# Performance work log

Hardware: AMD Instinct MI355X
Metric: run time of the kernel (lower is better)

The kernel has to match this reference:

```python
import jax, jax.numpy as jnp
import numpy as np

B, S, D, H, DK, L, DFF, V = 64, 128, 512, 8, 64, 6, 2048, 72
AH = 2          # heads of the internal mask-generating attention encoder (hard-coded n_heads=2)
PRECET = 0.2    # fraction of lowest-attention prefix tokens to mask
NEG = -1e9


def pos_enc(s, d):
    pos = jnp.arange(s, dtype=jnp.float32)[:, None]
    div = jnp.exp(jnp.arange(0, d, 2, dtype=jnp.float32) * (-np.log(10000.0) / d))
    pe = jnp.zeros((s, d), jnp.float32)
    pe = pe.at[:, 0::2].set(jnp.sin(pos * div))
    pe = pe.at[:, 1::2].set(jnp.cos(pos * div))
    return pe


def ln(x, eps=1e-5):  # LayerNorm with default (identity) affine params, as in the source
    m = x.mean(-1, keepdims=True)
    v = ((x - m) ** 2).mean(-1, keepdims=True)
    return (x - m) / jnp.sqrt(v + eps)


def attn_block(x, pad, WQ, WK, WV, WO, heads):
    b, s, _ = x.shape
    dk = WQ.shape[1] // heads
    q = (x @ WQ).reshape(b, s, heads, dk).transpose(0, 2, 1, 3)
    k = (x @ WK).reshape(b, s, heads, dk).transpose(0, 2, 1, 3)
    v = (x @ WV).reshape(b, s, heads, dk).transpose(0, 2, 1, 3)
    scores = jnp.einsum('bhqd,bhkd->bhqk', q, k) / np.sqrt(dk)
    scores = jnp.where(pad[:, None, None, :], NEG, scores)
    attn = jax.nn.softmax(scores, axis=-1)
    ascore = attn.sum(axis=2)                                   # [b, h, s] column sums
    ctx = jnp.einsum('bhqk,bhkd->bqhd', attn, v).reshape(b, s, heads * dk)
    return ln(ctx @ WO + x), attn, ascore


def ffn_block(x, W1, W2):
    return ln(jax.nn.relu(x @ W1) @ W2 + x)


def encode(x, pad, tWQ, tWK, tWV, tFC, tF1, tF2):
    def step(h, p):
        WQ, WK, WV, WO, W1, W2 = p
        h, _, asc = attn_block(h, pad, WQ, WK, WV, WO, H)
        h = ffn_block(h, W1, W2)
        return h, asc.sum(axis=1)                               # sum over heads -> [b, s]
    h, scores = jax.lax.scan(step, x, (tWQ, tWK, tWV, tFC, tF1, tF2))
    return h, scores                                            # scores: [L, b, s]


def creat_mask(col, tokens):
    # col[i, j] == 0 exactly iff token j is pad (softmax of -1e9 underflows to 0).
    b, s = tokens.shape
    iszero = col == 0.0
    has = iszero.any(axis=1)
    j0 = jnp.where(has, jnp.argmax(iszero, axis=1), s)          # first pad position
    kk = jnp.where(has, jnp.ceil(PRECET * j0.astype(jnp.float32)).astype(jnp.int32), 0)
    idx = jnp.arange(s)
    vals = jnp.where(idx[None, :] < j0[:, None], col, jnp.inf)
    ranks = jnp.argsort(jnp.argsort(vals, axis=1), axis=1)      # rank 0 = smallest attention
    keep = (ranks >= kk[:, None]).astype(tokens.dtype)
    return tokens * keep


def pre_head(x, pW1, pb1, pW2, pb2, pW3, pb3):
    x = jax.nn.relu(x @ pW1 + pb1)
    x = jax.nn.relu(x @ pW2 + pb2)
    return x @ pW3 + pb3


def setup_inputs():
    key = jax.random.key(0)
    ks = jax.random.split(key, 18)
    g = lambda k, shp: jax.random.normal(k, shp, jnp.float32) * 0.02
    return {
        'tokens': jax.random.randint(ks[0], (B, S), 0, V, dtype=jnp.int32),
        'emb': g(ks[1], (V, D)),
        'aWQ': g(ks[2], (D, AH * DK)), 'aWK': g(ks[3], (D, AH * DK)), 'aWV': g(ks[4], (D, AH * DK)),
        'aFC': g(ks[5], (AH * DK, D)), 'aF1': g(ks[6], (D, DFF)), 'aF2': g(ks[7], (DFF, D)),
        'tWQ': g(ks[8], (L, D, H * DK)), 'tWK': g(ks[9], (L, D, H * DK)), 'tWV': g(ks[10], (L, D, H * DK)),
        'tFC': g(ks[11], (L, H * DK, D)), 'tF1': g(ks[12], (L, D, DFF)), 'tF2': g(ks[13], (L, DFF, D)),
        'pW1': g(ks[14], (D * S, 1024)), 'pb1': jnp.zeros((1024,), jnp.float32),
        'pW2': g(ks[15], (1024, 512)), 'pb2': jnp.zeros((512,), jnp.float32),
        'pW3': g(ks[16], (512, 128)), 'pb3': jnp.zeros((128,), jnp.float32),
    }


def reference(tokens, emb, aWQ, aWK, aWV, aFC, aF1, aF2,
              tWQ, tWK, tWV, tFC, tF1, tF2,
              pW1, pb1, pW2, pb2, pW3, pb3):
    pe = pos_enc(S, D)[None]
    pad = tokens == 0
    x = emb[tokens] + pe
    # 1-layer / 2-head mask-generating encoder; only its attn matrix is consumed downstream
    _, mattn, _ = attn_block(x, pad, aWQ, aWK, aWV, aFC, AH)
    col = mattn.sum(axis=1).sum(axis=1)                         # heads then queries -> [B, S]
    mtok = creat_mask(col, tokens)
    xm = emb[mtok] + pe
    h, scores = encode(x, pad, tWQ, tWK, tWV, tFC, tF1, tF2)
    hm, _ = encode(xm, mtok == 0, tWQ, tWK, tWV, tFC, tF1, tF2)
    out1 = pre_head(h.reshape(B, -1), pW1, pb1, pW2, pb2, pW3, pb3)
    outm = pre_head(hm.reshape(B, -1), pW1, pb1, pW2, pb2, pW3, pb3)
    return tokens, out1, mtok, outm, scores
```

## Files before the change

kernel.cpp:

```cpp
#include <hip/hip_runtime.h>
#include <hip/hip_bf16.h>
#include <math.h>

using u16 = unsigned short;
using u32 = unsigned int;

constexpr int B   = 64;
constexpr int S   = 128;
constexpr int D   = 512;
constexpr int H   = 8;
constexpr int DK  = 64;
constexpr int L   = 6;
constexpr int DFF = 2048;
constexpr int AH  = 2;
constexpr int BS  = B * S;
constexpr int BS2 = 2 * BS;

constexpr long OUT_TOK    = 0;
constexpr long OUT_OUT1   = 8192;
constexpr long OUT_MTOK   = 16384;
constexpr long OUT_OUTM   = 24576;
constexpr long OUT_SCORES = 32768;

constexpr long OFF_PE   = 0;
constexpr long OFF_ASC  = 65536;
constexpr long OFF_COLP = 196608;
constexpr long OFF_MTOK = 212992;
constexpr long OFF_X    = 221184;
constexpr long OFF_XB   = 8609792;
constexpr long OFF_QB   = 12804096;
constexpr long OFF_KB   = 16998400;
constexpr long OFF_VB   = 21192704;
constexpr long OFF_TB   = 25387008;
constexpr long OFF_W    = 42164224;
constexpr long WSTRIDE  = 3145728;

typedef __attribute__((ext_vector_type(8))) short bf16x8;
typedef __attribute__((ext_vector_type(4))) float f32x4;

__device__ __forceinline__ float b2f(u16 u) {
    union { u32 i; float f; } v; v.i = ((u32)u) << 16; return v.f;
}
__device__ __forceinline__ u16 f2b(float f) {
    union { float f; u32 i; } v; v.f = f;
    u32 r = v.i + 0x7fffu + ((v.i >> 16) & 1u);
    return (u16)(r >> 16);
}

#define GLOAD_LDS16(g, l) __builtin_amdgcn_global_load_lds(                        \
    (const __attribute__((address_space(1))) u32*)(const void*)(g),               \
    (__attribute__((address_space(3))) u32*)(void*)(l), 16, 0, 0)

__global__ void pe_kernel(float* __restrict__ pe) {
    int idx = blockIdx.x * 256 + threadIdx.x;
    if (idx >= S * (D / 2)) return;
    int s = idx >> 8;
    int i = idx & 255;
    const float CPE = (float)(-9.210340371976184 / 512.0);
    float div = expf((float)(2 * i) * CPE);
    float ang = (float)s * div;
    pe[(long)s * D + 2 * i]     = sinf(ang);
    pe[(long)s * D + 2 * i + 1] = cosf(ang);
}

__global__ void embed_dual(const int* __restrict__ toks, const float* __restrict__ emb,
                           const float* __restrict__ pe, float* __restrict__ x,
                           u16* __restrict__ xb) {
    int i8 = blockIdx.x * 256 + threadIdx.x;
    if (i8 >= BS * D / 8) return;
    int row = i8 >> 6;
    int c8  = i8 & 63;
    int s   = row & (S - 1);
    int t   = toks[row];
    float4 e0 = *(const float4*)(emb + (long)t * D + c8 * 8);
    float4 e1 = *(const float4*)(emb + (long)t * D + c8 * 8 + 4);
    float4 p0 = *(const float4*)(pe + (long)s * D + c8 * 8);
    float4 p1 = *(const float4*)(pe + (long)s * D + c8 * 8 + 4);
    float4 o0, o1;
    o0.x = e0.x + p0.x; o0.y = e0.y + p0.y; o0.z = e0.z + p0.z; o0.w = e0.w + p0.w;
    o1.x = e1.x + p1.x; o1.y = e1.y + p1.y; o1.z = e1.z + p1.z; o1.w = e1.w + p1.w;
    *(float4*)(x + (long)i8 * 8)     = o0;
    *(float4*)(x + (long)i8 * 8 + 4) = o1;
    u16 u[8] = {f2b(o0.x), f2b(o0.y), f2b(o0.z), f2b(o0.w), f2b(o1.x), f2b(o1.y), f2b(o1.z), f2b(o1.w)};
    *(uint4*)(xb + (long)i8 * 8) = *(uint4*)u;
}

__global__ __launch_bounds__(256)
void wconv_all(const float* __restrict__ tWQ, const float* __restrict__ tWK,
               const float* __restrict__ tWV, const float* __restrict__ tFC,
               const float* __restrict__ tF1, const float* __restrict__ tF2,
               u16* __restrict__ wAll) {
    __shared__ float t[32][33];
    const int lyr = blockIdx.x / 3072;
    const int bid = blockIdx.x % 3072;
    u16* base = wAll + (long)lyr * WSTRIDE;
    const float* src; u16* dst; int KK, NN, tk, tn;
    if (bid < 1024) {
        int which = bid >> 8, tt = bid & 255;
        src = (which == 0 ? tWQ : which == 1 ? tWK : which == 2 ? tWV : tFC) + (long)lyr * D * D;
        dst = base + (long)which * 262144;
        KK = 512; NN = 512; tk = tt >> 4; tn = tt & 15;
    } else if (bid < 2048) {
        int tt = bid - 1024;
        src = tF1 + (long)lyr * D * DFF; dst = base + 1048576;
        KK = 512; NN = 2048; tk = tt >> 6; tn = tt & 63;
    } else {
        int tt = bid - 2048;
        src = tF2 + (long)lyr * DFF * D; dst = base + 2097152;
        KK = 2048; NN = 512; tk = tt >> 4; tn = tt & 15;
    }
    int ty = threadIdx.x >> 5, tx = threadIdx.x & 31;
    #pragma unroll
    for (int i = 0; i < 4; i++)
        t[ty + i * 8][tx] = src[(long)(tk * 32 + ty + i * 8) * NN + tn * 32 + tx];
    __syncthreads();
    #pragma unroll
    for (int i = 0; i < 4; i++)
        dst[(long)(tn * 32 + ty + i * 8) * KK + tk * 32 + tx] = f2b(t[tx][ty + i * 8]);
}

template<int EPI, int OUTB>
__device__ __forceinline__ void gemm_core(
        const u16* __restrict__ A, const u16* __restrict__ Wt,
        float* C, u16* Cb, const float* __restrict__ X,
        int M, int N, int K, int m0, int n0) {
    __shared__ u16 As[128 * 32];
    __shared__ u16 Bs[128 * 32];
    const int tid = threadIdx.x;
    const int w = tid >> 6, l = tid & 63;
    const int wr = (w >> 1) * 64, wc = (w & 1) * 64;
    f32x4 acc[4][4];
    #pragma unroll
    for (int i = 0; i < 4; i++)
        #pragma unroll
        for (int j = 0; j < 4; j++) { f32x4 z = {0.f, 0.f, 0.f, 0.f}; acc[i][j] = z; }

    const int srow = w * 32 + (l >> 2);
    const int scol = (l & 3) * 8;
    const u16* gA = A + (long)(m0 + srow) * K + scol;
    const u16* gB = Wt + (long)(n0 + srow) * K + scol;
    u16* lA0 = As + w * 1024;
    u16* lA1 = As + w * 1024 + 512;
    u16* lB0 = Bs + w * 1024;
    u16* lB1 = Bs + w * 1024 + 512;

    for (int k0 = 0; k0 < K; k0 += 32) {
        GLOAD_LDS16(gA + k0,               lA0);
        GLOAD_LDS16(gA + (long)16 * K + k0, lA1);
        GLOAD_LDS16(gB + k0,               lB0);
        GLOAD_LDS16(gB + (long)16 * K + k0, lB1);
        __syncthreads();
        bf16x8 aF[4], bF[4];
        #pragma unroll
        for (int mi = 0; mi < 4; mi++)
            aF[mi] = *(const bf16x8*)(As + (wr + mi * 16 + (l & 15)) * 32 + (l >> 4) * 8);
        #pragma unroll
        for (int ni = 0; ni < 4; ni++)
            bF[ni] = *(const bf16x8*)(Bs + (wc + ni * 16 + (l & 15)) * 32 + (l >> 4) * 8);
        #pragma unroll
        for (int mi = 0; mi < 4; mi++)
            #pragma unroll
            for (int ni = 0; ni < 4; ni++)
                acc[mi][ni] = __builtin_amdgcn_mfma_f32_16x16x32_bf16(aF[mi], bF[ni], acc[mi][ni], 0, 0, 0);
        __syncthreads();
    }

    #pragma unroll
    for (int mi = 0; mi < 4; mi++) {
        #pragma unroll
        for (int ni = 0; ni < 4; ni++) {
            const int col = n0 + wc + ni * 16 + (l & 15);
            #pragma unroll
            for (int r = 0; r < 4; r++) {
                const int row = m0 + wr + mi * 16 + (l >> 4) * 4 + r;
                const long idx = (long)row * N + col;
                float v = acc[mi][ni][r];
                if (EPI == 1) v += X[idx];
                if (EPI == 2) v = fmaxf(v, 0.0f);
                if (OUTB) Cb[idx] = f2b(v);
                else      C[idx]  = v;
            }
        }
    }
}

__global__ __launch_bounds__(256)
void gemm_qkv_b(const u16* __restrict__ A, const u16* wq, const u16* wk, const u16* wv,
                u16* qb, u16* kb, u16* vb, int M, int N, int K) {
    const u16* Wt = blockIdx.z == 0 ? wq : blockIdx.z == 1 ? wk : wv;
    u16* Cb       = blockIdx.z == 0 ? qb : blockIdx.z == 1 ? kb : vb;
    gemm_core<0, 1>(A, Wt, nullptr, Cb, nullptr, M, N, K, blockIdx.x * 128, blockIdx.y * 128);
}
__global__ __launch_bounds__(256)
void gemm_relu_b(const u16* __restrict__ A, const u16* __restrict__ Wt,
                 u16* Cb, int M, int N, int K) {
    gemm_core<2, 1>(A, Wt, nullptr, Cb, nullptr, M, N, K, blockIdx.x * 128, blockIdx.y * 128);
}

__global__ __launch_bounds__(512)
void gemm_ln(const u16* __restrict__ A, const u16* __restrict__ Wt,
             float* x, u16* __restrict__ xb, int K) {
    __shared__ u16 As[64 * 32];
    __shared__ u16 Bs[512 * 32];
    __shared__ float redS[64][9];
    __shared__ float redQ[64][9];
    __shared__ float meanS[64], invS[64];
    const int m0 = blockIdx.x * 64;
    const int tid = threadIdx.x;
    const int w = tid >> 6, l = tid & 63;
    const int wc = w * 64;

    f32x4 acc[4][4];
    #pragma unroll
    for (int i = 0; i < 4; i++)
        #pragma unroll
        for (int j = 0; j < 4; j++) { f32x4 z = {0.f, 0.f, 0.f, 0.f}; acc[i][j] = z; }

    const int scol = (l & 3) * 8;
    const u16* gA = A + (long)(m0 + w * 16 + (l >> 2)) * K + scol;
    const u16* gB = Wt + (long)(w * 64 + (l >> 2)) * K + scol;
    u16* lA = As + (w * 16) * 32;
    u16* lB = Bs + (w * 64) * 32;

    for (int k0 = 0; k0 < K; k0 += 32) {
        if (w < 4) GLOAD_LDS16(gA + k0, lA);
        #pragma unroll
        for (int j = 0; j < 4; j++)
            GLOAD_LDS16(gB + (long)j * 16 * K + k0, lB + j * 16 * 32);
        __syncthreads();
        bf16x8 aF[4], bF[4];
        #pragma unroll
        for (int mi = 0; mi < 4; mi++)
            aF[mi] = *(const bf16x8*)(As + (mi * 16 + (l & 15)) * 32 + (l >> 4) * 8);
        #pragma unroll
        for (int ni = 0; ni < 4; ni++)
            bF[ni] = *(const bf16x8*)(Bs + (wc + ni * 16 + (l & 15)) * 32 + (l >> 4) * 8);
        #pragma unroll
        for (int mi = 0; mi < 4; mi++)
            #pragma unroll
            for (int ni = 0; ni < 4; ni++)
                acc[mi][ni] = __builtin_amdgcn_mfma_f32_16x16x32_bf16(aF[mi], bF[ni], acc[mi][ni], 0, 0, 0);
        __syncthreads();
    }

    #pragma unroll
    for (int mi = 0; mi < 4; mi++)
        #pragma unroll
        for (int r = 0; r < 4; r++) {
            const int row = mi * 16 + (l >> 4) * 4 + r;
            float s = 0.0f, q = 0.0f;
            #pragma unroll
            for (int ni = 0; ni < 4; ni++) {
                const int col = wc + ni * 16 + (l & 15);
                float v = acc[mi][ni][r] + x[(long)(m0 + row) * D + col];
                acc[mi][ni][r] = v;
                s += v; q += v * v;
            }
            s += __shfl_xor(s, 1); s += __shfl_xor(s, 2); s += __shfl_xor(s, 4); s += __shfl_xor(s, 8);
            q += __shfl_xor(q, 1); q += __shfl_xor(q, 2); q += __shfl_xor(q, 4); q += __shfl_xor(q, 8);
            if ((l & 15) == 0) { redS[row][w] = s; redQ[row][w] = q; }
        }
    __syncthreads();
    if (tid < 64) {
        float s = 0.0f, q = 0.0f;
        #pragma unroll
        for (int ww = 0; ww < 8; ww++) { s += redS[tid][ww]; q += redQ[tid][ww]; }
        float mean = s * (1.0f / 512.0f);
        float var  = q * (1.0f / 512.0f) - mean * mean;
        meanS[tid] = mean;
        invS[tid]  = 1.0f / sqrtf(var + 1e-5f);
    }
    __syncthreads();
    #pragma unroll
    for (int mi = 0; mi < 4; mi++)
        #pragma unroll
        for (int r = 0; r < 4; r++) {
            const int row = mi * 16 + (l >> 4) * 4 + r;
            const float mn = meanS[row], iv = invS[row];
            #pragma unroll
            for (int ni = 0; ni < 4; ni++) {
                const int col = wc + ni * 16 + (l & 15);
                const long idx = (long)(m0 + row) * D + col;
                float o = (acc[mi][ni][r] - mn) * iv;
                x[idx]  = o;
                xb[idx] = f2b(o);
            }
        }
}

template<int EPI>
__global__ __launch_bounds__(256)
void gemm64(const float* __restrict__ A, const float* __restrict__ W,
            float* C, const float* X, int M, int N, int K) {
    __shared__ float As[32][68];
    __shared__ float Ws[32][64];
    const int m0 = blockIdx.x * 64, n0 = blockIdx.y * 64;
    const int tid  = threadIdx.x;
    const int tr   = tid >> 4, tc = tid & 15;
    const int arow = tid >> 3, acg = tid & 7;
    const int wrow = tid >> 4, wcg = tid & 15;
    float acc[4][4] = {};
    for (int k0 = 0; k0 < K; k0 += 32) {
        float4 a0 = *(const float4*)(A + (long)(m0 + arow) * K + k0 + acg * 4);
        float4 a1 = *(const float4*)(A + (long)(m0 + arow + 32) * K + k0 + acg * 4);
        float4 w0 = *(const float4*)(W + (long)(k0 + wrow) * N + n0 + wcg * 4);
        float4 w1 = *(const float4*)(W + (long)(k0 + wrow + 16) * N + n0 + wcg * 4);
        As[acg * 4 + 0][arow] = a0.x; As[acg * 4 + 1][arow] = a0.y;
        As[acg * 4 + 2][arow] = a0.z; As[acg * 4 + 3][arow] = a0.w;
        As[acg * 4 + 0][arow + 32] = a1.x; As[acg * 4 + 1][arow + 32] = a1.y;
        As[acg * 4 + 2][arow + 32] = a1.z; As[acg * 4 + 3][arow + 32] = a1.w;
        *(float4*)&Ws[wrow][wcg * 4]      = w0;
        *(float4*)&Ws[wrow + 16][wcg * 4] = w1;
        __syncthreads();
        #pragma unroll
        for (int kk = 0; kk < 32; kk++) {
            float4 av = *(const float4*)&As[kk][tr * 4];
            float4 bv = *(const float4*)&Ws[kk][tc * 4];
            acc[0][0] += av.x * bv.x; acc[0][1] += av.x * bv.y; acc[0][2] += av.x * bv.z; acc[0][3] += av.x * bv.w;
            acc[1][0] += av.y * bv.x; acc[1][1] += av.y * bv.y; acc[1][2] += av.y * bv.z; acc[1][3] += av.y * bv.w;
            acc[2][0] += av.z * bv.x; acc[2][1] += av.z * bv.y; acc[2][2] += av.z * bv.z; acc[2][3] += av.z * bv.w;
            acc[3][0] += av.w * bv.x; acc[3][1] += av.w * bv.y; acc[3][2] += av.w * bv.z; acc[3][3] += av.w * bv.w;
        }
        __syncthreads();
    }
    #pragma unroll
    for (int i = 0; i < 4; i++) {
        int row = m0 + tr * 4 + i;
        #pragma unroll
        for (int j = 0; j < 4; j++) {
            int col = n0 + tc * 4 + j;
            long idx = (long)row * N + col;
            float v = acc[i][j];
            if (EPI == 1) v += X[idx];
            if (EPI == 3 || EPI == 4) v += X[col];
            if (EPI == 2 || EPI == 4) v = fmaxf(v, 0.0f);
            C[idx] = v;
        }
    }
}

__global__ __launch_bounds__(256)
void gemm64_qkv(const float* __restrict__ A,
                const float* __restrict__ WQ, const float* __restrict__ WK, const float* __restrict__ WV,
                float* q, float* k, float* v, int M, int N, int K) {
    __shared__ float As[32][68];
    __shared__ float Ws[32][64];
    const float* W = (blockIdx.z == 0) ? WQ : (blockIdx.z == 1) ? WK : WV;
    float*       C = (blockIdx.z == 0) ? q  : (blockIdx.z == 1) ? k  : v;
    const int m0 = blockIdx.x * 64, n0 = blockIdx.y * 64;
    const int tid  = threadIdx.x;
    const int tr   = tid >> 4, tc = tid & 15;
    const int arow = tid >> 3, acg = tid & 7;
    const int wrow = tid >> 4, wcg = tid & 15;
    float acc[4][4] = {};
    for (int k0 = 0; k0 < K; k0 += 32) {
        float4 a0 = *(const float4*)(A + (long)(m0 + arow) * K + k0 + acg * 4);
        float4 a1 = *(const float4*)(A + (long)(m0 + arow + 32) * K + k0 + acg * 4);
        float4 w0 = *(const float4*)(W + (long)(k0 + wrow) * N + n0 + wcg * 4);
        float4 w1 = *(const float4*)(W + (long)(k0 + wrow + 16) * N + n0 + wcg * 4);
        As[acg * 4 + 0][arow] = a0.x; As[acg * 4 + 1][arow] = a0.y;
        As[acg * 4 + 2][arow] = a0.z; As[acg * 4 + 3][arow] = a0.w;
        As[acg * 4 + 0][arow + 32] = a1.x; As[acg * 4 + 1][arow + 32] = a1.y;
        As[acg * 4 + 2][arow + 32] = a1.z; As[acg * 4 + 3][arow + 32] = a1.w;
        *(float4*)&Ws[wrow][wcg * 4]      = w0;
        *(float4*)&Ws[wrow + 16][wcg * 4] = w1;
        __syncthreads();
        #pragma unroll
        for (int kk = 0; kk < 32; kk++) {
            float4 av = *(const float4*)&As[kk][tr * 4];
            float4 bv = *(const float4*)&Ws[kk][tc * 4];
            acc[0][0] += av.x * bv.x; acc[0][1] += av.x * bv.y; acc[0][2] += av.x * bv.z; acc[0][3] += av.x * bv.w;
            acc[1][0] += av.y * bv.x; acc[1][1] += av.y * bv.y; acc[1][2] += av.y * bv.z; acc[1][3] += av.y * bv.w;
            acc[2][0] += av.z * bv.x; acc[2][1] += av.z * bv.y; acc[2][2] += av.z * bv.z; acc[2][3] += av.z * bv.w;
            acc[3][0] += av.w * bv.x; acc[3][1] += av.w * bv.y; acc[3][2] += av.w * bv.z; acc[3][3] += av.w * bv.w;
        }
        __syncthreads();
    }
    #pragma unroll
    for (int i = 0; i < 4; i++)
        #pragma unroll
        for (int j = 0; j < 4; j++)
            C[(long)(m0 + tr * 4 + i) * N + n0 + tc * 4 + j] = acc[i][j];
}

__global__ __launch_bounds__(256)
void gemm_ph1(const u16* __restrict__ Ah, const u16* __restrict__ Ahm,
              const float* __restrict__ W, float* __restrict__ P, int KC) {
    constexpr int N = 1024, K = 65536;
    __shared__ u16 As[128 * 32];
    __shared__ u16 Bs[128 * 32];
    const int n0 = blockIdx.x * 128;
    const int kbeg = blockIdx.y * KC;
    const int tid = threadIdx.x;
    const int w = tid >> 6, l = tid & 63;
    const int wr = w * 32;
    const int nl = tid >> 1, seg = tid & 1;
    const u16* aptr = (nl < 64 ? Ah + (long)nl * K : Ahm + (long)(nl - 64) * K) + seg * 16;
    const float* wcol = W + n0 + nl;

    f32x4 acc[2][8];
    #pragma unroll
    for (int mi = 0; mi < 2; mi++)
        #pragma unroll
        for (int ni = 0; ni < 8; ni++) { f32x4 z = {0.f, 0.f, 0.f, 0.f}; acc[mi][ni] = z; }

    for (int ks = 0; ks < KC; ks += 32) {
        const int k0 = kbeg + ks;
        uint4 a0 = *(const uint4*)(aptr + k0);
        uint4 a1 = *(const uint4*)(aptr + k0 + 8);
        float wv[16];
        #pragma unroll
        for (int j = 0; j < 16; j++)
            wv[j] = wcol[(long)(k0 + seg * 16 + j) * N];
        __syncthreads();
        *(uint4*)(As + nl * 32 + seg * 16)     = a0;
        *(uint4*)(As + nl * 32 + seg * 16 + 8) = a1;
        u32 pk[8];
        #pragma unroll
        for (int j = 0; j < 8; j++)
            pk[j] = (u32)f2b(wv[2 * j]) | ((u32)f2b(wv[2 * j + 1]) << 16);
        *(uint4*)(Bs + nl * 32 + seg * 16)     = *(uint4*)&pk[0];
        *(uint4*)(Bs + nl * 32 + seg * 16 + 8) = *(uint4*)&pk[4];
        __syncthreads();
        bf16x8 aF0 = *(const bf16x8*)(As + (wr + (l & 15)) * 32 + (l >> 4) * 8);
        bf16x8 aF1 = *(const bf16x8*)(As + (wr + 16 + (l & 15)) * 32 + (l >> 4) * 8);
        #pragma unroll
        for (int ni = 0; ni < 8; ni++) {
            bf16x8 bF = *(const bf16x8*)(Bs + (ni * 16 + (l & 15)) * 32 + (l >> 4) * 8);
            acc[0][ni] = __builtin_amdgcn_mfma_f32_16x16x32_bf16(aF0, bF, acc[0][ni], 0, 0, 0);
            acc[1][ni] = __builtin_amdgcn_mfma_f32_16x16x32_bf16(aF1, bF, acc[1][ni], 0, 0, 0);
        }
    }
    float* Pz = P + (long)blockIdx.y * 128 * N;
    #pragma unroll
    for (int mi = 0; mi < 2; mi++)
        #pragma unroll
        for (int ni = 0; ni < 8; ni++) {
            const int col = n0 + ni * 16 + (l & 15);
            #pragma unroll
            for (int r = 0; r < 4; r++)
                Pz[(long)(wr + mi * 16 + (l >> 4) * 4 + r) * N + col] = acc[mi][ni][r];
        }
}

__global__ __launch_bounds__(128)
void attn_kernel(const float* __restrict__ Q, const float* __restrict__ K,
                 const int* __restrict__ toks, float* __restrict__ colsum, int Hn) {
    __shared__ float sc[S][129];
    __shared__ float KV[S][DK];
    __shared__ int   padS[S];
    const int b = blockIdx.x / Hn;
    const int h = blockIdx.x % Hn;
    const int stride = Hn * DK;
    const int tid = threadIdx.x;

    for (int idx = tid; idx < S * DK; idx += 128) {
        int r = idx >> 6, c = idx & 63;
        KV[r][c] = K[(long)(b * S + r) * stride + h * DK + c];
    }
    padS[tid] = (toks[b * S + tid] == 0) ? 1 : 0;
    float qreg[DK];
    {
        const float* qp = Q + (long)(b * S + tid) * stride + h * DK;
        #pragma unroll
        for (int i = 0; i < 16; i++) {
            float4 t4 = *(const float4*)(qp + i * 4);
            qreg[i * 4 + 0] = t4.x; qreg[i * 4 + 1] = t4.y;
            qreg[i * 4 + 2] = t4.z; qreg[i * 4 + 3] = t4.w;
        }
    }
    __syncthreads();
    for (int k = 0; k < S; k++) {
        float s = 0.0f;
        #pragma unroll
        for (int d4 = 0; d4 < 16; d4++) {
            float4 kv = *(const float4*)&KV[k][d4 * 4];
            s += qreg[d4 * 4 + 0] * kv.x + qreg[d4 * 4 + 1] * kv.y
               + qreg[d4 * 4 + 2] * kv.z + qreg[d4 * 4 + 3] * kv.w;
        }
        sc[tid][k] = padS[k] ? -1e9f : (s * 0.125f);
    }
    float mx = -INFINITY;
    for (int k = 0; k < S; k++) mx = fmaxf(mx, sc[tid][k]);
    float sum = 0.0f;
    for (int k = 0; k < S; k++) { float e = expf(sc[tid][k] - mx); sc[tid][k] = e; sum += e; }
    for (int k = 0; k < S; k++) sc[tid][k] = sc[tid][k] / sum;
    __syncthreads();
    {
        double a = 0.0;
        for (int q2 = 0; q2 < S; q2++) a += (double)sc[q2][tid];
        colsum[(long)(b * Hn + h) * S + tid] = (float)a;
    }
}

__global__ __launch_bounds__(256)
void attn_mfma_kernel(u16* qb, const u16* __restrict__ kb, const u16* __restrict__ vb,
                      const int* __restrict__ toks, const int* __restrict__ mtok,
                      float* __restrict__ colsum) {
    __shared__ u16 pool[18432];
    __shared__ u16 Vt[64 * 136];
    __shared__ float colsLds[4][128];
    __shared__ u32 padF[128];
    u16* Qs = pool;
    u16* Ks = pool + 9216;
    u16* Ps = pool;

    const int gb = blockIdx.x >> 3, h = blockIdx.x & 7;
    const int tid = threadIdx.x;
    const int w = tid >> 6, l = tid & 63;
    const long base = (long)gb * S * D + h * 64;
    const int* tsrc = (gb < B) ? (toks + (long)gb * S) : (mtok + (long)(gb - B) * S);

    for (int j = tid; j < 1024; j += 256) {
        int r = j >> 3, c = j & 7;
        uint4 uq = *(const uint4*)(qb + base + (long)r * D + c * 8);
        uint4 uk = *(const uint4*)(kb + base + (long)r * D + c * 8);
        uint4 uv = *(const uint4*)(vb + base + (long)r * D + c * 8);
        *(uint4*)(Qs + r * 72 + c * 8) = uq;
        *(uint4*)(Ks + r * 72 + c * 8) = uk;
        u16 vv[8]; *(uint4*)vv = uv;
        #pragma unroll
        for (int t = 0; t < 8; t++) Vt[(c * 8 + t) * 136 + r] = vv[t];
    }
    if (tid < 128) padF[tid] = (tsrc[tid] == 0) ? 1u : 0u;
    __syncthreads();

    const int rowB = w * 32;
    f32x4 acc[2][8];
    #pragma unroll
    for (int mi = 0; mi < 2; mi++)
        #pragma unroll
        for (int ni = 0; ni < 8; ni++) { f32x4 z = {0.f, 0.f, 0.f, 0.f}; acc[mi][ni] = z; }
    #pragma unroll
    for (int ks = 0; ks < 2; ks++) {
        bf16x8 a0 = *(const bf16x8*)(Qs + (rowB + (l & 15)) * 72 + ks * 32 + (l >> 4) * 8);
        bf16x8 a1 = *(const bf16x8*)(Qs + (rowB + 16 + (l & 15)) * 72 + ks * 32 + (l >> 4) * 8);
        #pragma unroll
        for (int ni = 0; ni < 8; ni++) {
            bf16x8 bv = *(const bf16x8*)(Ks + (ni * 16 + (l & 15)) * 72 + ks * 32 + (l >> 4) * 8);
            acc[0][ni] = __builtin_amdgcn_mfma_f32_16x16x32_bf16(a0, bv, acc[0][ni], 0, 0, 0);
            acc[1][ni] = __builtin_amdgcn_mfma_f32_16x16x32_bf16(a1, bv, acc[1][ni], 0, 0, 0);
        }
    }
    float pf[8];
    #pragma unroll
    for (int ni = 0; ni < 8; ni++) pf[ni] = padF[ni * 16 + (l & 15)] ? 1.0f : 0.0f;
    #pragma unroll
    for (int mi = 0; mi < 2; mi++)
        #pragma unroll
        for (int ni = 0; ni < 8; ni++)
            #pragma unroll
            for (int r = 0; r < 4; r++) {
                float v = acc[mi][ni][r] * 0.125f;
                acc[mi][ni][r] = (pf[ni] != 0.0f) ? -1e9f : v;
            }
    #pragma unroll
    for (int mi = 0; mi < 2; mi++)
        #pragma unroll
        for (int r = 0; r < 4; r++) {
            float m = -INFINITY;
            #pragma unroll
            for (int ni = 0; ni < 8; ni++) m = fmaxf(m, acc[mi][ni][r]);
            m = fmaxf(m, __shfl_xor(m, 1)); m = fmaxf(m, __shfl_xor(m, 2));
            m = fmaxf(m, __shfl_xor(m, 4)); m = fmaxf(m, __shfl_xor(m, 8));
            float s = 0.0f;
            #pragma unroll
            for (int ni = 0; ni < 8; ni++) { float e = expf(acc[mi][ni][r] - m); acc[mi][ni][r] = e; s += e; }
            s += __shfl_xor(s, 1); s += __shfl_xor(s, 2);
            s += __shfl_xor(s, 4); s += __shfl_xor(s, 8);
            float inv = 1.0f / s;
            #pragma unroll
            for (int ni = 0; ni < 8; ni++) acc[mi][ni][r] *= inv;
        }
    float cs[8];
    #pragma unroll
    for (int ni = 0; ni < 8; ni++) {
        float s = 0.0f;
        #pragma unroll
        for (int mi = 0; mi < 2; mi++)
            #pragma unroll
            for (int r = 0; r < 4; r++) s += acc[mi][ni][r];
        s += __shfl_xor(s, 16); s += __shfl_xor(s, 32);
        cs[ni] = s;
    }
    __syncthreads();
    if (l < 16)
        #pragma unroll
        for (int ni = 0; ni < 8; ni++) colsLds[w][ni * 16 + l] = cs[ni];
    #pragma unroll
    for (int mi = 0; mi < 2; mi++)
        #pragma unroll
        for (int ni = 0; ni < 8; ni++)
            #pragma unroll
            for (int r = 0; r < 4; r++)
                Ps[(rowB + mi * 16 + (l >> 4) * 4 + r) * 136 + ni * 16 + (l & 15)] =
                    f2b(acc[mi][ni][r]);
    __syncthreads();
    if (tid < 128) {
        float s = colsLds[0][tid] + colsLds[1][tid] + colsLds[2][tid] + colsLds[3][tid];
        colsum[((long)gb * H + h) * S + tid] = s;
    }
    f32x4 o[2][4];
    #pragma unroll
    for (int mi = 0; mi < 2; mi++)
        #pragma unroll
        for (int n = 0; n < 4; n++) { f32x4 z = {0.f, 0.f, 0.f, 0.f}; o[mi][n] = z; }
    #pragma unroll
    for (int ks = 0; ks < 4; ks++) {
        bf16x8 p0 = *(const bf16x8*)(Ps + (rowB + (l & 15)) * 136 + ks * 32 + (l >> 4) * 8);
        bf16x8 p1 = *(const bf16x8*)(Ps + (rowB + 16 + (l & 15)) * 136 + ks * 32 + (l >> 4) * 8);
        #pragma unroll
        for (int n = 0; n < 4; n++) {
            bf16x8 bv = *(const bf16x8*)(Vt + (n * 16 + (l & 15)) * 136 + ks * 32 + (l >> 4) * 8);
            o[0][n] = __builtin_amdgcn_mfma_f32_16x16x32_bf16(p0, bv, o[0][n], 0, 0, 0);
            o[1][n] = __builtin_amdgcn_mfma_f32_16x16x32_bf16(p1, bv, o[1][n], 0, 0, 0);
        }
    }
    #pragma unroll
    for (int mi = 0; mi < 2; mi++)
        #pragma unroll
        for (int n = 0; n < 4; n++) {
            const int col = n * 16 + (l & 15);
            #pragma unroll
            for (int r = 0; r < 4; r++) {
                const int row = rowB + mi * 16 + (l >> 4) * 4 + r;
                qb[base + (long)row * D + col] = f2b(o[mi][n][r]);
            }
        }
}

__global__ __launch_bounds__(128)
void creat_mask_kernel(const float* __restrict__ colpart, const int* __restrict__ toks,
                       int* __restrict__ mtok, float* __restrict__ out) {
    __shared__ float colS[S];
    __shared__ int   j0s, kks;
    const int b = blockIdx.x, j = threadIdx.x;
    float c = colpart[(long)(b * AH + 0) * S + j] + colpart[(long)(b * AH + 1) * S + j];
    colS[j] = c;
    int tk = toks[b * S + j];
    __syncthreads();
    if (j == 0) {
        int j0 = S;
        for (int i = 0; i < S; i++) if (colS[i] == 0.0f) { j0 = i; break; }
        int kk = (j0 < S) ? (int)ceilf(0.2f * (float)j0) : 0;
        j0s = j0; kks = kk;
    }
    __syncthreads();
    const int j0 = j0s, kk = kks;
    float vj = (j < j0) ? colS[j] : INFINITY;
    int rank = 0;
    for (int i = 0; i < S; i++) {
        float vi = (i < j0) ? colS[i] : INFINITY;
        if (vi < vj || (vi == vj && i < j)) rank++;
    }
    int mt = (rank >= kk) ? tk : 0;
    mtok[b * S + j] = mt;
    out[OUT_TOK + b * S + j]  = (float)tk;
    out[OUT_MTOK + b * S + j] = (float)mt;
}

__global__ void score_reduce_kernel(const float* __restrict__ ascorep, float* __restrict__ dst) {
    int idx = blockIdx.x * 256 + threadIdx.x;
    if (idx >= B * S) return;
    int b = idx >> 7, j = idx & 127;
    float s = 0.0f;
    for (int h = 0; h < H; h++) s += ascorep[(long)(b * H + h) * S + j];
    dst[idx] = s;
}

__global__ void reduce1_kernel(const float* __restrict__ parts, const float* __restrict__ b1,
                               float* __restrict__ o) {
    int idx = blockIdx.x * 256 + threadIdx.x;
    if (idx >= 128 * 1024) return;
    float s = 0.0f;
    for (int z = 0; z < 64; z++) s += parts[(long)z * 128 * 1024 + idx];
    s += b1[idx & 1023];
    o[idx] = fmaxf(s, 0.0f);
}

__global__ void pack_out_kernel(const float* __restrict__ ph3, float* __restrict__ out) {
    int idx = blockIdx.x * 256 + threadIdx.x;
    if (idx >= 128 * 128) return;
    int row = idx >> 7, col = idx & 127;
    long base = (row < 64) ? (OUT_OUT1 + (long)row * 128) : (OUT_OUTM + (long)(row - 64) * 128);
    out[base + col] = ph3[idx];
}

extern "C" void kernel_launch(void* const* d_in, const int* in_sizes, int n_in,
                              void* d_out, int out_size, void* d_ws, size_t ws_size,
                              hipStream_t stream) {
    const int*   toks = (const int*)d_in[0];
    const float* emb  = (const float*)d_in[1];
    const float* aWQ  = (const float*)d_in[2];
    const float* aWK  = (const float*)d_in[3];
    const float* tWQ  = (const float*)d_in[8];
    const float* tWK  = (const float*)d_in[9];
    const float* tWV  = (const float*)d_in[10];
    const float* tFC  = (const float*)d_in[11];
    const float* tF1  = (const float*)d_in[12];
    const float* tF2  = (const float*)d_in[13];
    const float* pW1  = (const float*)d_in[14];
    const float* pb1  = (const float*)d_in[15];
    const float* pW2  = (const float*)d_in[16];
    const float* pb2  = (const float*)d_in[17];
    const float* pW3  = (const float*)d_in[18];
    const float* pb3  = (const float*)d_in[19];
    float* out = (float*)d_out;

    float* ws   = (float*)d_ws;
    float* pe   = ws + OFF_PE;
    float* ascp = ws + OFF_ASC;
    float* colp = ws + OFF_COLP;
    int*   mtok = (int*)(ws + OFF_MTOK);
    float* x    = ws + OFF_X;
    u16*   xb   = (u16*)(ws + OFF_XB);
    u16*   qb   = (u16*)(ws + OFF_QB);
    u16*   kb   = (u16*)(ws + OFF_KB);
    u16*   vb   = (u16*)(ws + OFF_VB);
    u16*   tb   = (u16*)(ws + OFF_TB);
    u16*   wAll = (u16*)(ws + OFF_W);

    float* maq   = ws + OFF_TB;
    float* mak   = maq + (long)BS * 128;
    float* parts = ws + OFF_TB;
    float* ph1o  = parts + 8388608;
    float* ph2o  = ph1o + 131072;
    float* ph3o  = ph2o + 65536;

    pe_kernel<<<128, 256, 0, stream>>>(pe);
    wconv_all<<<6 * 3072, 256, 0, stream>>>(tWQ, tWK, tWV, tFC, tF1, tF2, wAll);
    embed_dual<<<2048, 256, 0, stream>>>(toks, emb, pe, x, xb);

    gemm64_qkv<<<dim3(BS / 64, 2, 2), 256, 0, stream>>>(
        x, aWQ, aWK, nullptr, maq, mak, nullptr, BS, AH * DK, D);
    attn_kernel<<<B * AH, 128, 0, stream>>>(maq, mak, toks, colp, AH);
    creat_mask_kernel<<<B, 128, 0, stream>>>(colp, toks, mtok, out);
    embed_dual<<<2048, 256, 0, stream>>>(mtok, emb, pe, x + (long)BS * D, xb + (long)BS * D);

    for (int l = 0; l < L; l++) {
        const u16* wq = wAll + (long)l * WSTRIDE;
        const u16* wk = wq + 262144;
        const u16* wv = wq + 524288;
        const u16* wo = wq + 786432;
        const u16* w1 = wq + 1048576;
        const u16* w2 = wq + 2097152;
        gemm_qkv_b<<<dim3(BS2 / 128, D / 128, 3), 256, 0, stream>>>(
            xb, wq, wk, wv, qb, kb, vb, BS2, D, D);
        attn_mfma_kernel<<<2 * B * H, 256, 0, stream>>>(qb, kb, vb, toks, mtok, ascp);
        score_reduce_kernel<<<32, 256, 0, stream>>>(ascp, out + OUT_SCORES + (long)l * BS);
        gemm_ln<<<BS2 / 64, 512, 0, stream>>>(qb, wo, x, xb, D);
        gemm_relu_b<<<dim3(BS2 / 128, DFF / 128), 256, 0, stream>>>(xb, w1, tb, BS2, DFF, D);
        gemm_ln<<<BS2 / 64, 512, 0, stream>>>(tb, w2, x, xb, DFF);
    }

    gemm_ph1<<<dim3(8, 64), 256, 0, stream>>>(xb, xb + (long)BS * D, pW1, parts, 1024);
    reduce1_kernel<<<512, 256, 0, stream>>>(parts, pb1, ph1o);
    gemm64<4><<<dim3(2, 8), 256, 0, stream>>>(ph1o, pW2, ph2o, pb2, 128, 512, 1024);
    gemm64<3><<<dim3(2, 2), 256, 0, stream>>>(ph2o, pW3, ph3o, pb3, 128, 128, 512);
    pack_out_kernel<<<64, 256, 0, stream>>>(ph3o, out);
}
```

Baseline: 1.809 ms.

## Retile fused GEMM+LayerNorm to 32-row blocks and skip final fp32 store

The full-row GEMM+residual+LayerNorm kernel now uses 32-row blocks of 256 threads, with each of 4 warps covering 128 output columns, instead of 64-row blocks of 512 threads with 64 columns per warp. This doubles the grid to 512 blocks, which should fill the GPU better, at the cost of loading the full 512-row weight tile into LDS twice as often per output row. The last layer's FFN LayerNorm also skips writing the fp32 residual stream, since only the bf16 copy is read by the prediction head.

```diff
diff --git a/kernel.cpp b/kernel.cpp
--- a/kernel.cpp
+++ b/kernel.cpp
@@ -197,60 +197,58 @@
     gemm_core<2, 1>(A, Wt, nullptr, Cb, nullptr, M, N, K, blockIdx.x * 128, blockIdx.y * 128);
 }
 
-__global__ __launch_bounds__(512)
-void gemm_ln(const u16* __restrict__ A, const u16* __restrict__ Wt,
-             float* x, u16* __restrict__ xb, int K) {
-    __shared__ u16 As[64 * 32];
+__global__ __launch_bounds__(256)
+void gemm_ln2(const u16* __restrict__ A, const u16* __restrict__ Wt,
+              float* x, u16* __restrict__ xb, int K, int writeX) {
+    __shared__ u16 As[32 * 32];
     __shared__ u16 Bs[512 * 32];
-    __shared__ float redS[64][9];
-    __shared__ float redQ[64][9];
-    __shared__ float meanS[64], invS[64];
-    const int m0 = blockIdx.x * 64;
+    __shared__ float redS[32][5];
+    __shared__ float redQ[32][5];
+    __shared__ float meanS[32], invS[32];
+    const int m0 = blockIdx.x * 32;
     const int tid = threadIdx.x;
     const int w = tid >> 6, l = tid & 63;
-    const int wc = w * 64;
-
-    f32x4 acc[4][4];
-    #pragma unroll
-    for (int i = 0; i < 4; i++)
-        #pragma unroll
-        for (int j = 0; j < 4; j++) { f32x4 z = {0.f, 0.f, 0.f, 0.f}; acc[i][j] = z; }
-
+    const int wc = w * 128;
+
+    f32x4 acc[2][8];
+    #pragma unroll
+    for (int i = 0; i < 2; i++)
+        #pragma unroll
+        for (int j = 0; j < 8; j++) { f32x4 z = {0.f, 0.f, 0.f, 0.f}; acc[i][j] = z; }
+
+    const int srow = l >> 2;
     const int scol = (l & 3) * 8;
-    const u16* gA = A + (long)(m0 + w * 16 + (l >> 2)) * K + scol;
-    const u16* gB = Wt + (long)(w * 64 + (l >> 2)) * K + scol;
+    const u16* gB = Wt + (long)(wc + srow) * K + scol;
+    u16* lB = Bs + wc * 32;
+    const u16* gA = A + (long)(m0 + w * 16 + srow) * K + scol;
     u16* lA = As + (w * 16) * 32;
-    u16* lB = Bs + (w * 64) * 32;
 
     for (int k0 = 0; k0 < K; k0 += 32) {
-        if (w < 4) GLOAD_LDS16(gA + k0, lA);
-        #pragma unroll
-        for (int j = 0; j < 4; j++)
+        if (w < 2) GLOAD_LDS16(gA + k0, lA);
+        #pragma unroll
+        for (int j = 0; j < 8; j++)
             GLOAD_LDS16(gB + (long)j * 16 * K + k0, lB + j * 16 * 32);
         __syncthreads();
-        bf16x8 aF[4], bF[4];
-        #pragma unroll
-        for (int mi = 0; mi < 4; mi++)
-            aF[mi] = *(const bf16x8*)(As + (mi * 16 + (l & 15)) * 32 + (l >> 4) * 8);
-        #pragma unroll
-        for (int ni = 0; ni < 4; ni++)
-            bF[ni] = *(const bf16x8*)(Bs + (wc + ni * 16 + (l & 15)) * 32 + (l >> 4) * 8);
-        #pragma unroll
-        for (int mi = 0; mi < 4; mi++)
-            #pragma unroll
-            for (int ni = 0; ni < 4; ni++)
-                acc[mi][ni] = __builtin_amdgcn_mfma_f32_16x16x32_bf16(aF[mi], bF[ni], acc[mi][ni], 0, 0, 0);
-        __syncthreads();
-    }
-
-    #pragma unroll
-    for (int mi = 0; mi < 4; mi++)
+        bf16x8 aF[2];
+        aF[0] = *(const bf16x8*)(As + ((l & 15)) * 32 + (l >> 4) * 8);
+        aF[1] = *(const bf16x8*)(As + (16 + (l & 15)) * 32 + (l >> 4) * 8);
+        #pragma unroll
+        for (int ni = 0; ni < 8; ni++) {
+            bf16x8 bF = *(const bf16x8*)(Bs + (wc + ni * 16 + (l & 15)) * 32 + (l >> 4) * 8);
+            acc[0][ni] = __builtin_amdgcn_mfma_f32_16x16x32_bf16(aF[0], bF, acc[0][ni], 0, 0, 0);
+            acc[1][ni] = __builtin_amdgcn_mfma_f32_16x16x32_bf16(aF[1], bF, acc[1][ni], 0, 0, 0);
+        }
+        __syncthreads();
+    }
+
+    #pragma unroll
+    for (int mi = 0; mi < 2; mi++)
         #pragma unroll
         for (int r = 0; r < 4; r++) {
             const int row = mi * 16 + (l >> 4) * 4 + r;
             float s = 0.0f, q = 0.0f;
             #pragma unroll
-            for (int ni = 0; ni < 4; ni++) {
+            for (int ni = 0; ni < 8; ni++) {
                 const int col = wc + ni * 16 + (l & 15);
                 float v = acc[mi][ni][r] + x[(long)(m0 + row) * D + col];
                 acc[mi][ni][r] = v;
@@ -261,10 +259,10 @@
             if ((l & 15) == 0) { redS[row][w] = s; redQ[row][w] = q; }
         }
     __syncthreads();
-    if (tid < 64) {
+    if (tid < 32) {
         float s = 0.0f, q = 0.0f;
         #pragma unroll
-        for (int ww = 0; ww < 8; ww++) { s += redS[tid][ww]; q += redQ[tid][ww]; }
+        for (int ww = 0; ww < 4; ww++) { s += redS[tid][ww]; q += redQ[tid][ww]; }
         float mean = s * (1.0f / 512.0f);
         float var  = q * (1.0f / 512.0f) - mean * mean;
         meanS[tid] = mean;
@@ -272,17 +270,17 @@
     }
     __syncthreads();
     #pragma unroll
-    for (int mi = 0; mi < 4; mi++)
+    for (int mi = 0; mi < 2; mi++)
         #pragma unroll
         for (int r = 0; r < 4; r++) {
             const int row = mi * 16 + (l >> 4) * 4 + r;
             const float mn = meanS[row], iv = invS[row];
             #pragma unroll
-            for (int ni = 0; ni < 4; ni++) {
+            for (int ni = 0; ni < 8; ni++) {
                 const int col = wc + ni * 16 + (l & 15);
                 const long idx = (long)(m0 + row) * D + col;
                 float o = (acc[mi][ni][r] - mn) * iv;
-                x[idx]  = o;
+                if (writeX) x[idx] = o;
                 xb[idx] = f2b(o);
             }
         }
@@ -748,9 +746,9 @@
             xb, wq, wk, wv, qb, kb, vb, BS2, D, D);
         attn_mfma_kernel<<<2 * B * H, 256, 0, stream>>>(qb, kb, vb, toks, mtok, ascp);
         score_reduce_kernel<<<32, 256, 0, stream>>>(ascp, out + OUT_SCORES + (long)l * BS);
-        gemm_ln<<<BS2 / 64, 512, 0, stream>>>(qb, wo, x, xb, D);
+        gemm_ln2<<<BS2 / 32, 256, 0, stream>>>(qb, wo, x, xb, D, 1);
         gemm_relu_b<<<dim3(BS2 / 128, DFF / 128), 256, 0, stream>>>(xb, w1, tb, BS2, DFF, D);
-        gemm_ln<<<BS2 / 64, 512, 0, stream>>>(tb, w2, x, xb, DFF);
+        gemm_ln2<<<BS2 / 32, 256, 0, stream>>>(tb, w2, x, xb, DFF, l < L - 1);
     }
 
     gemm_ph1<<<dim3(8, 64), 256, 0, stream>>>(xb, xb + (long)BS * D, pW1, parts, 1024);
```

Measured after the change: 1.739 ms. 3.9% less time.
